# Kernel tuning notes

Hardware: AMD Instinct MI355X
Metric: run time of the kernel (lower is better)

The kernel has to match this reference:

```python
import jax, jax.numpy as jnp
import numpy as np

B, S, D, E = 4096, 32, 512, 512


def setup_inputs() -> dict:
    key = jax.random.key(0)
    kx, kq, kk, kv = jax.random.split(key, 4)
    return {
        "x": jax.random.normal(kx, (B, S * D), dtype=jnp.float32),
        "Q": jax.random.normal(kq, (S, D, E), dtype=jnp.float32),
        "K": jax.random.normal(kk, (S, D, E), dtype=jnp.float32),
        "V": jax.random.normal(kv, (S, D, E), dtype=jnp.float32),
    }


def reference(x, Q, K, V):
    # x: [B, S*D] -> [B, S, D]; per-segment projections via batched einsum
    b = x.shape[0]
    xs = x.reshape(b, S, D)
    q = jnp.einsum("bsd,sde->bse", xs, Q)  # [B, S, E]
    k = jnp.einsum("bsd,sde->bse", xs, K)
    v = jnp.einsum("bsd,sde->bse", xs, V)
    scores = jnp.sum(q * k, axis=-1)  # [B, S]
    # L2-normalize scores across segments (matches torch norm(dim=1))
    weights = scores / jnp.linalg.norm(scores, axis=1, keepdims=True)
    # weighted sum of per-segment value vectors
    y = jnp.einsum("bs,bse->be", weights, v)  # [B, E]
    return y
```

## Files before the change

kernel.cpp:

```cpp
#include <hip/hip_runtime.h>
#include <hip/hip_bf16.h>
#include <math.h>


typedef __attribute__((ext_vector_type(8))) short s8v;
typedef __attribute__((ext_vector_type(4))) float f4v;

#define MFMA_BF16(a, b, c) __builtin_amdgcn_mfma_f32_16x16x32_bf16((a), (b), (c), 0, 0, 0)

constexpr int NB = 4096;
constexpr int NS = 32;
constexpr int ND = 512;
constexpr int NE = 512;
constexpr int SD = NS * ND;

__device__ __forceinline__ short f2bf(float f) {
  union { float f; unsigned u; } v; v.f = f;
  unsigned r = v.u + 0x7fffu + ((v.u >> 16) & 1u);
  return (short)(r >> 16);
}
__device__ __forceinline__ float bf2f(short h) {
  union { unsigned u; float f; } v; v.u = ((unsigned)(unsigned short)h) << 16;
  return v.f;
}
__device__ __forceinline__ s8v cvt8(const float* p) {
  s8v r;
#pragma unroll
  for (int i = 0; i < 8; ++i) r[i] = f2bf(p[i]);
  return r;
}

__device__ __forceinline__ void gload16(const void* g, void* l) {
  __builtin_amdgcn_global_load_lds(
      (const __attribute__((address_space(1))) unsigned int*)g,
      (__attribute__((address_space(3))) unsigned int*)l, 16, 0, 0);
}

__global__ __launch_bounds__(256) void k_castx(const float* __restrict__ x,
                                               short* __restrict__ xb,
                                               float* __restrict__ scores) {
  size_t gtid = (size_t)blockIdx.x * 256 + threadIdx.x;
  if (gtid < (size_t)NB * NS / 4) {
    f4v z = (f4v)0.0f;
    *(f4v*)(scores + gtid * 4) = z;
  }
  size_t i = gtid * 8;
  f4v a = *(const f4v*)(x + i);
  f4v b = *(const f4v*)(x + i + 4);
  s8v o;
#pragma unroll
  for (int u = 0; u < 4; ++u) { o[u] = f2bf(a[u]); o[4 + u] = f2bf(b[u]); }
  *(s8v*)(xb + i) = o;
}

__global__ __launch_bounds__(256) void k_misc(const float* __restrict__ V,
                                              short* __restrict__ Vt,
                                              const float* __restrict__ Kw,
                                              const float* __restrict__ Qw,
                                              short* __restrict__ G) {
  __shared__ __align__(16) char smem[36864];
  int bid = blockIdx.x;
  int tid = threadIdx.x;

  if (bid >= 512) {
    float (*t)[65] = (float(*)[65])smem;
    int t2 = bid - 512;
    int k0 = (t2 & 255) * 64;
    int e0 = (t2 >> 8) * 64;
#pragma unroll
    for (int i = 0; i < 16; ++i) {
      int idx = tid + 256 * i;
      int r = idx >> 6, c = idx & 63;
      t[r][c] = V[(size_t)(k0 + r) * NE + e0 + c];
    }
    __syncthreads();
#pragma unroll
    for (int i = 0; i < 16; ++i) {
      int idx = tid + 256 * i;
      int e = idx >> 6, k = idx & 63;
      Vt[(size_t)(e0 + e) * SD + k0 + k] = f2bf(t[k][e]);
    }
  } else {
    int t3 = bid;
    int s = t3 >> 4;
    int tm = (t3 >> 2) & 3, tn = t3 & 3;
    const float* A = Kw + (size_t)s * ND * NE + (size_t)tm * 128 * NE;
    const float* B = Qw + (size_t)s * ND * NE + (size_t)tn * 128 * NE;
    short* Gs = G + (size_t)s * ND * ND;

    s8v (*lsA)[9] = (s8v(*)[9])smem;
    s8v (*lsB)[9] = (s8v(*)[9])(smem + 18432);

    int lane = tid & 63, wid = tid >> 6;
    int wr = wid >> 1, wc = wid & 1;
    int lhi = lane >> 4, llo = lane & 15;

    float ra[4][8], rb[4][8];
    f4v acc[4][4];
#pragma unroll
    for (int i = 0; i < 4; ++i)
#pragma unroll
      for (int j = 0; j < 4; ++j) acc[i][j] = (f4v)0.0f;

    auto loadRegs = [&](int k0) {
#pragma unroll
      for (int i = 0; i < 4; ++i) {
        int c = tid + 256 * i; int row = c >> 3, k8 = c & 7;
        const float* p = A + (size_t)row * NE + k0 + k8 * 8;
        *(f4v*)&ra[i][0] = *(const f4v*)p;
        *(f4v*)&ra[i][4] = *(const f4v*)(p + 4);
        const float* q = B + (size_t)row * NE + k0 + k8 * 8;
        *(f4v*)&rb[i][0] = *(const f4v*)q;
        *(f4v*)&rb[i][4] = *(const f4v*)(q + 4);
      }
    };
    auto writeLds = [&]() {
#pragma unroll
      for (int i = 0; i < 4; ++i) {
        int c = tid + 256 * i; int row = c >> 3, k8 = c & 7;
        lsA[row][k8] = cvt8(ra[i]);
        lsB[row][k8] = cvt8(rb[i]);
      }
    };

    loadRegs(0);
    writeLds();
    for (int kt = 0; kt < 8; ++kt) {
      __syncthreads();
      if (kt + 1 < 8) loadRegs((kt + 1) * 64);
#pragma unroll
      for (int kk = 0; kk < 2; ++kk) {
        s8v af[4], bq[4];
#pragma unroll
        for (int i = 0; i < 4; ++i) af[i] = lsA[wr * 64 + i * 16 + llo][kk * 4 + lhi];
#pragma unroll
        for (int j = 0; j < 4; ++j) bq[j] = lsB[wc * 64 + j * 16 + llo][kk * 4 + lhi];
#pragma unroll
        for (int i = 0; i < 4; ++i)
#pragma unroll
          for (int j = 0; j < 4; ++j) acc[i][j] = MFMA_BF16(af[i], bq[j], acc[i][j]);
      }
      __syncthreads();
      if (kt + 1 < 8) writeLds();
    }

#pragma unroll
    for (int i = 0; i < 4; ++i)
#pragma unroll
      for (int r = 0; r < 4; ++r) {
        int row = tm * 128 + wr * 64 + i * 16 + lhi * 4 + r;
#pragma unroll
        for (int j = 0; j < 4; ++j) {
          int col = tn * 128 + wc * 64 + j * 16 + llo;
          Gs[(size_t)row * ND + col] = f2bf(acc[i][j][r]);
        }
      }
  }
}

__global__ __launch_bounds__(256) void k_symm(const short* __restrict__ G,
                                              short* __restrict__ U) {
  int s = blockIdx.y;
  int kt = blockIdx.x >> 3, nt = blockIdx.x & 7;
  const short* Gs = G + (size_t)s * ND * ND;
  short* Us = U + (size_t)s * ND * ND;
  int k0 = kt * 64, n0 = nt * 64;
  int tid = threadIdx.x;
  int r = tid >> 2, cb = (tid & 3) * 16;

  if (kt > nt) {
    s8v z = (s8v)(short)0;
    *(s8v*)&Us[(size_t)(k0 + r) * ND + n0 + cb] = z;
    *(s8v*)&Us[(size_t)(k0 + r) * ND + n0 + cb + 8] = z;
    return;
  }

  __shared__ float tt[64][65];
  {
    const short* src = &Gs[(size_t)(n0 + r) * ND + k0 + cb];
    s8v a = *(const s8v*)src;
    s8v b = *(const s8v*)(src + 8);
#pragma unroll
    for (int u = 0; u < 8; ++u) { tt[r][cb + u] = bf2f(a[u]); tt[r][cb + 8 + u] = bf2f(b[u]); }
  }
  __syncthreads();
  {
    const short* src = &Gs[(size_t)(k0 + r) * ND + n0 + cb];
    s8v a = *(const s8v*)src;
    s8v b = *(const s8v*)(src + 8);
    s8v oa, ob;
#pragma unroll
    for (int u = 0; u < 8; ++u) {
      int k = k0 + r;
      int n1 = n0 + cb + u, n2 = n0 + cb + 8 + u;
      float g1 = bf2f(a[u]), g2 = bf2f(b[u]);
      float v1 = (k < n1) ? (g1 + tt[cb + u][r]) : ((k == n1) ? g1 : 0.f);
      float v2 = (k < n2) ? (g2 + tt[cb + 8 + u][r]) : ((k == n2) ? g2 : 0.f);
      oa[u] = f2bf(v1); ob[u] = f2bf(v2);
    }
    short* dst = &Us[(size_t)(k0 + r) * ND + n0 + cb];
    *(s8v*)dst = oa;
    *(s8v*)(dst + 8) = ob;
  }
}

__global__ __launch_bounds__(512, 4) void k_scores(const short* __restrict__ xb,
                                                   const short* __restrict__ U,
                                                   float* __restrict__ scores) {
  int t = blockIdx.x;
  int swz = (t & 7) * 256 + (t >> 3);
  int s = swz >> 6;
  int mt = (swz >> 2) & 15;
  int nt = swz & 3;
  int b0 = mt * 256, n0 = nt * 128;
  const short* Asrc = xb + (size_t)b0 * SD + s * ND;
  const short* Bt = U + (size_t)s * ND * ND + (size_t)n0 * ND;

  __shared__ __align__(16) short lsA[256 * 64];
  __shared__ __align__(16) short lsB[128 * 64];

  int tid = threadIdx.x;
  int lane = tid & 63, wid = tid >> 6;
  int wr = wid >> 1, wc = wid & 1;
  int lhi = lane >> 4, llo = lane & 15;
  int lrow = lane >> 3, lcol = (lane & 7) * 8;

  f4v acc[4][4];
#pragma unroll
  for (int i = 0; i < 4; ++i)
#pragma unroll
    for (int j = 0; j < 4; ++j) acc[i][j] = (f4v)0.0f;

  for (int kt = 2 * nt; kt < 8; ++kt) {
    int k0 = kt * 64;
#pragma unroll
    for (int c = 0; c < 4; ++c) {
      int chunk = wid * 4 + c;
      int row = chunk * 8 + lrow;
      gload16(Asrc + (size_t)row * SD + k0 + lcol, (char*)lsA + chunk * 1024);
    }
#pragma unroll
    for (int c = 0; c < 2; ++c) {
      int chunk = wid * 2 + c;
      int row = chunk * 8 + lrow;
      gload16(Bt + (size_t)row * ND + k0 + lcol, (char*)lsB + chunk * 1024);
    }
    __syncthreads();
    const s8v* fA = (const s8v*)lsA;
    const s8v* fB = (const s8v*)lsB;
#pragma unroll
    for (int kk = 0; kk < 2; ++kk) {
      s8v af[4], bq[4];
#pragma unroll
      for (int i = 0; i < 4; ++i) af[i] = fA[(wr * 64 + i * 16 + llo) * 8 + kk * 4 + lhi];
#pragma unroll
      for (int j = 0; j < 4; ++j) bq[j] = fB[(wc * 64 + j * 16 + llo) * 8 + kk * 4 + lhi];
#pragma unroll
      for (int i = 0; i < 4; ++i)
#pragma unroll
        for (int j = 0; j < 4; ++j) acc[i][j] = MFMA_BF16(af[i], bq[j], acc[i][j]);
    }
    __syncthreads();
  }

#pragma unroll
  for (int i = 0; i < 4; ++i)
#pragma unroll
    for (int r = 0; r < 4; ++r) {
      int rowl = wr * 64 + i * 16 + lhi * 4 + r;
      int b = b0 + rowl;
      const short* xr = xb + (size_t)b * SD + s * ND + n0 + wc * 64;
      float v = 0.f;
#pragma unroll
      for (int j = 0; j < 4; ++j) v += bf2f(xr[j * 16 + llo]) * acc[i][j][r];
      v += __shfl_xor(v, 1);
      v += __shfl_xor(v, 2);
      v += __shfl_xor(v, 4);
      v += __shfl_xor(v, 8);
      if (llo == 0) atomicAdd(&scores[b * NS + s], v);
    }
}

__global__ __launch_bounds__(256) void k_weights(const float* __restrict__ scores,
                                                 float* __restrict__ w) {
  int b = blockIdx.x * 256 + threadIdx.x;
  float sq = 0.f, sc[NS];
#pragma unroll
  for (int s = 0; s < NS; ++s) { sc[s] = scores[b * NS + s]; sq += sc[s] * sc[s]; }
  float inv = 1.0f / sqrtf(sq);
#pragma unroll
  for (int s = 0; s < NS; ++s) w[b * NS + s] = sc[s] * inv;
}

__global__ __launch_bounds__(256, 3) void k_out(const short* __restrict__ xb,
                                                const float* __restrict__ wts,
                                                const short* __restrict__ Vt,
                                                float* __restrict__ y_part) {
  int t = blockIdx.x;
  int kg = t & 7;
  int nt = (t >> 3) & 1;
  int mt = t >> 4;
  int b0 = mt * 64, n0 = nt * 256;
  const short* Asrc = xb + (size_t)b0 * SD + kg * 2048;
  const short* Bsrc = Vt + (size_t)n0 * SD + kg * 2048;
  float* yp = y_part + (size_t)kg * NB * NE;

  __shared__ __align__(16) short lsA[64 * 64];
  __shared__ __align__(16) short lsB[256 * 64];

  int tid = threadIdx.x;
  int lane = tid & 63, wid = tid >> 6;
  int lhi = lane >> 4, llo = lane & 15;

  int arow0 = tid >> 3;
  int arow1 = 32 + (tid >> 3);
  int acb = (tid & 7) * 8;

  f4v acc[4][4];
#pragma unroll
  for (int i = 0; i < 4; ++i)
#pragma unroll
    for (int j = 0; j < 4; ++j) acc[i][j] = (f4v)0.0f;

  for (int sl = 0; sl < 4; ++sl) {
    int s = kg * 4 + sl;
    float w0 = wts[(b0 + arow0) * NS + s];
    float w1 = wts[(b0 + arow1) * NS + s];
#pragma unroll 1
    for (int k8 = 0; k8 < 8; ++k8) {
      int k0 = sl * 512 + k8 * 64;
#pragma unroll
      for (int c = 0; c < 8; ++c) {
        int chunk = wid * 8 + c;
        int idx = chunk * 64 + lane;
        gload16(Bsrc + (size_t)(idx >> 3) * SD + k0 + (idx & 7) * 8,
                (char*)lsB + chunk * 1024);
      }
      s8v a0 = *(const s8v*)(Asrc + (size_t)arow0 * SD + k0 + acb);
      s8v a1 = *(const s8v*)(Asrc + (size_t)arow1 * SD + k0 + acb);
      s8v o0, o1;
#pragma unroll
      for (int u = 0; u < 8; ++u) {
        o0[u] = f2bf(bf2f(a0[u]) * w0);
        o1[u] = f2bf(bf2f(a1[u]) * w1);
      }
      *(s8v*)((char*)lsA + tid * 16) = o0;
      *(s8v*)((char*)lsA + 4096 + tid * 16) = o1;
      __syncthreads();
      const s8v* fA = (const s8v*)lsA;
      const s8v* fB = (const s8v*)lsB;
#pragma unroll
      for (int kk = 0; kk < 2; ++kk) {
        s8v af[4], bq[4];
#pragma unroll
        for (int i = 0; i < 4; ++i) af[i] = fA[(i * 16 + llo) * 8 + kk * 4 + lhi];
#pragma unroll
        for (int j = 0; j < 4; ++j) bq[j] = fB[(wid * 64 + j * 16 + llo) * 8 + kk * 4 + lhi];
#pragma unroll
        for (int i = 0; i < 4; ++i)
#pragma unroll
          for (int j = 0; j < 4; ++j) acc[i][j] = MFMA_BF16(af[i], bq[j], acc[i][j]);
      }
      __syncthreads();
    }
  }

#pragma unroll
  for (int i = 0; i < 4; ++i)
#pragma unroll
    for (int r = 0; r < 4; ++r) {
      int row = b0 + i * 16 + lhi * 4 + r;
#pragma unroll
      for (int j = 0; j < 4; ++j) {
        int col = n0 + wid * 64 + j * 16 + llo;
        yp[(size_t)row * NE + col] = acc[i][j][r];
      }
    }
}

__global__ __launch_bounds__(256) void k_reduce(const float* __restrict__ y_part,
                                                float* __restrict__ y) {
  size_t f = ((size_t)blockIdx.x * 256 + threadIdx.x) * 4;
  f4v acc = *(const f4v*)(y_part + f);
#pragma unroll
  for (int kg = 1; kg < 8; ++kg)
    acc += *(const f4v*)(y_part + (size_t)kg * NB * NE + f);
  *(f4v*)(y + f) = acc;
}

extern "C" void kernel_launch(void* const* d_in, const int* in_sizes, int n_in,
                              void* d_out, int out_size, void* d_ws, size_t ws_size,
                              hipStream_t stream) {
  const float* x  = (const float*)d_in[0];
  const float* Qw = (const float*)d_in[1];
  const float* Kw = (const float*)d_in[2];
  const float* Vw = (const float*)d_in[3];
  float* y = (float*)d_out;

  char* ws = (char*)d_ws;
  short* xb     = (short*)ws;
  short* G      = (short*)(ws + (size_t)128 * 1024 * 1024);
  short* Vt     = (short*)(ws + (size_t)144 * 1024 * 1024);
  short* Ut     = (short*)(ws + (size_t)160 * 1024 * 1024);
  float* scores = (float*)(ws + (size_t)176 * 1024 * 1024);
  float* wts    = (float*)(ws + (size_t)176 * 1024 * 1024 + 512 * 1024);
  float* y_part = (float*)(ws + (size_t)192 * 1024 * 1024);

  k_castx<<<32768, 256, 0, stream>>>(x, xb, scores);
  k_misc<<<2560, 256, 0, stream>>>(Vw, Vt, Kw, Qw, G);
  k_symm<<<dim3(64, NS), 256, 0, stream>>>(G, Ut);
  k_scores<<<2048, 512, 0, stream>>>(xb, Ut, scores);
  k_weights<<<16, 256, 0, stream>>>(scores, wts);
  k_out<<<1024, 256, 0, stream>>>(xb, wts, Vt, y_part);
  k_reduce<<<2048, 256, 0, stream>>>(y_part, y);
}
```

Measured before the change: 351.3 us.

## Double-buffer LDS tiles in k_out to overlap global loads with MFMA

Result: slower. 381.9 us (+8.7%).

```diff
diff --git a/kernel.cpp b/kernel.cpp
--- a/kernel.cpp
+++ b/kernel.cpp
@@ -292,21 +292,21 @@
   for (int s = 0; s < NS; ++s) w[b * NS + s] = sc[s] * inv;
 }
 
-__global__ __launch_bounds__(256, 3) void k_out(const short* __restrict__ xb,
+__global__ __launch_bounds__(256, 2) void k_out(const short* __restrict__ xb,
                                                 const float* __restrict__ wts,
                                                 const short* __restrict__ Vt,
                                                 float* __restrict__ y_part) {
-  int t = blockIdx.x;
-  int kg = t & 7;
-  int nt = (t >> 3) & 1;
-  int mt = t >> 4;
+  int t0 = blockIdx.x;
+  int kg = t0 & 7;
+  int nt = (t0 >> 3) & 1;
+  int mt = t0 >> 4;
   int b0 = mt * 64, n0 = nt * 256;
   const short* Asrc = xb + (size_t)b0 * SD + kg * 2048;
   const short* Bsrc = Vt + (size_t)n0 * SD + kg * 2048;
   float* yp = y_part + (size_t)kg * NB * NE;
 
-  __shared__ __align__(16) short lsA[64 * 64];
-  __shared__ __align__(16) short lsB[256 * 64];
+  __shared__ __align__(16) short lsA[2][64 * 64];
+  __shared__ __align__(16) short lsB[2][256 * 64];
 
   int tid = threadIdx.x;
   int lane = tid & 63, wid = tid >> 6;
@@ -316,53 +316,77 @@
   int arow1 = 32 + (tid >> 3);
   int acb = (tid & 7) * 8;
 
+  float w0v[4], w1v[4];
+#pragma unroll
+  for (int sl = 0; sl < 4; ++sl) {
+    w0v[sl] = wts[(b0 + arow0) * NS + kg * 4 + sl];
+    w1v[sl] = wts[(b0 + arow1) * NS + kg * 4 + sl];
+  }
+
   f4v acc[4][4];
 #pragma unroll
   for (int i = 0; i < 4; ++i)
 #pragma unroll
     for (int j = 0; j < 4; ++j) acc[i][j] = (f4v)0.0f;
 
-  for (int sl = 0; sl < 4; ++sl) {
-    int s = kg * 4 + sl;
-    float w0 = wts[(b0 + arow0) * NS + s];
-    float w1 = wts[(b0 + arow1) * NS + s];
-#pragma unroll 1
-    for (int k8 = 0; k8 < 8; ++k8) {
-      int k0 = sl * 512 + k8 * 64;
-#pragma unroll
-      for (int c = 0; c < 8; ++c) {
-        int chunk = wid * 8 + c;
-        int idx = chunk * 64 + lane;
-        gload16(Bsrc + (size_t)(idx >> 3) * SD + k0 + (idx & 7) * 8,
-                (char*)lsB + chunk * 1024);
-      }
-      s8v a0 = *(const s8v*)(Asrc + (size_t)arow0 * SD + k0 + acb);
-      s8v a1 = *(const s8v*)(Asrc + (size_t)arow1 * SD + k0 + acb);
-      s8v o0, o1;
-#pragma unroll
-      for (int u = 0; u < 8; ++u) {
-        o0[u] = f2bf(bf2f(a0[u]) * w0);
-        o1[u] = f2bf(bf2f(a1[u]) * w1);
-      }
-      *(s8v*)((char*)lsA + tid * 16) = o0;
-      *(s8v*)((char*)lsA + 4096 + tid * 16) = o1;
-      __syncthreads();
-      const s8v* fA = (const s8v*)lsA;
-      const s8v* fB = (const s8v*)lsB;
-#pragma unroll
-      for (int kk = 0; kk < 2; ++kk) {
-        s8v af[4], bq[4];
-#pragma unroll
-        for (int i = 0; i < 4; ++i) af[i] = fA[(i * 16 + llo) * 8 + kk * 4 + lhi];
-#pragma unroll
-        for (int j = 0; j < 4; ++j) bq[j] = fB[(wid * 64 + j * 16 + llo) * 8 + kk * 4 + lhi];
-#pragma unroll
-        for (int i = 0; i < 4; ++i)
-#pragma unroll
-          for (int j = 0; j < 4; ++j) acc[i][j] = MFMA_BF16(af[i], bq[j], acc[i][j]);
-      }
-      __syncthreads();
-    }
+  auto bstage = [&](int buf, int k0) {
+#pragma unroll
+    for (int c = 0; c < 8; ++c) {
+      int chunk = wid * 8 + c;
+      int idx = chunk * 64 + lane;
+      gload16(Bsrc + (size_t)(idx >> 3) * SD + k0 + (idx & 7) * 8,
+              (char*)&lsB[buf][0] + chunk * 1024);
+    }
+  };
+  auto awrite = [&](int buf, s8v a0, s8v a1, float w0, float w1) {
+    s8v o0, o1;
+#pragma unroll
+    for (int u = 0; u < 8; ++u) {
+      o0[u] = f2bf(bf2f(a0[u]) * w0);
+      o1[u] = f2bf(bf2f(a1[u]) * w1);
+    }
+    *(s8v*)((char*)&lsA[buf][0] + tid * 16) = o0;
+    *(s8v*)((char*)&lsA[buf][0] + 4096 + tid * 16) = o1;
+  };
+
+  {
+    s8v a0 = *(const s8v*)(Asrc + (size_t)arow0 * SD + acb);
+    s8v a1 = *(const s8v*)(Asrc + (size_t)arow1 * SD + acb);
+    bstage(0, 0);
+    awrite(0, a0, a1, w0v[0], w1v[0]);
+  }
+  __syncthreads();
+
+#pragma unroll 2
+  for (int t = 0; t < 32; ++t) {
+    int cur = t & 1;
+    s8v na0, na1;
+    if (t + 1 < 32) {
+      int tn = t + 1;
+      int k0n = (tn >> 3) * 512 + (tn & 7) * 64;
+      na0 = *(const s8v*)(Asrc + (size_t)arow0 * SD + k0n + acb);
+      na1 = *(const s8v*)(Asrc + (size_t)arow1 * SD + k0n + acb);
+      bstage(cur ^ 1, k0n);
+    }
+    const s8v* fA = (const s8v*)&lsA[cur][0];
+    const s8v* fB = (const s8v*)&lsB[cur][0];
+#pragma unroll
+    for (int kk = 0; kk < 2; ++kk) {
+      s8v af[4], bq[4];
+#pragma unroll
+      for (int i = 0; i < 4; ++i) af[i] = fA[(i * 16 + llo) * 8 + kk * 4 + lhi];
+#pragma unroll
+      for (int j = 0; j < 4; ++j) bq[j] = fB[(wid * 64 + j * 16 + llo) * 8 + kk * 4 + lhi];
+#pragma unroll
+      for (int i = 0; i < 4; ++i)
+#pragma unroll
+        for (int j = 0; j < 4; ++j) acc[i][j] = MFMA_BF16(af[i], bq[j], acc[i][j]);
+    }
+    if (t + 1 < 32) {
+      int sln = (t + 1) >> 3;
+      awrite(cur ^ 1, na0, na1, w0v[sln], w1v[sln]);
+    }
+    __syncthreads();
   }
 
 #pragma unroll
```
